# Kernel optimization log

Measured on AMD Instinct MI355X. Metric: run time of the kernel, lower is better.

## Reference

```python
import jax, jax.numpy as jnp
import numpy as np

N = 100000
E = 1600000
G = 256
D_IN = 128
NEURON = 64
ATT_F = 8
K = 3
ALPHA = 0.1


def setup_inputs() -> dict:
    key = jax.random.key(0)
    ks = jax.random.split(key, 12)
    x = jax.random.normal(ks[0], (N, D_IN), dtype=jnp.float32)
    closeness_feature = jax.random.normal(ks[1], (N, ATT_F), dtype=jnp.float32)
    edge_index = jax.random.randint(ks[2], (2, E), 0, N, dtype=jnp.int32)
    batch = jnp.sort(jax.random.randint(ks[3], (N,), 0, G, dtype=jnp.int32))
    s = 0.05
    return {
        "x": x,
        "closeness_feature": closeness_feature,
        "edge_index": edge_index,
        "batch": batch,
        "num_graphs": G,
        "nn1_w": jax.random.normal(ks[4], (D_IN, NEURON), dtype=jnp.float32) * s,
        "nn1_b": jnp.zeros((NEURON,), dtype=jnp.float32),
        "close_w": jax.random.normal(ks[5], (ATT_F, 1), dtype=jnp.float32) * s,
        "close_b": jnp.zeros((1,), dtype=jnp.float32),
        "att1_w": jax.random.normal(ks[6], (NEURON, 16), dtype=jnp.float32) * s,
        "att1_b": jnp.zeros((16,), dtype=jnp.float32),
        "att2_w": jax.random.normal(ks[7], (16, 1), dtype=jnp.float32) * s,
        "att2_b": jnp.zeros((1,), dtype=jnp.float32),
    }


def _appnp(x, edge_index, n):
    # gcn_norm with self-loops: A_hat = D^{-1/2}(A+I)D^{-1/2}
    loop = jnp.arange(n, dtype=edge_index.dtype)
    src = jnp.concatenate([edge_index[0], loop])
    dst = jnp.concatenate([edge_index[1], loop])
    deg = jax.ops.segment_sum(jnp.ones_like(dst, dtype=x.dtype), dst, num_segments=n)
    dinv = jax.lax.rsqrt(deg)  # deg >= 1 due to self loops
    norm = (dinv[src] * dinv[dst])[:, None]  # [E+N, 1]
    h = x
    for _ in range(K):
        agg = jax.ops.segment_sum(norm * h[src], dst, num_segments=n)
        h = (1.0 - ALPHA) * agg + ALPHA * x
    return h


def reference(x, closeness_feature, edge_index, batch, num_graphs,
              nn1_w, nn1_b, close_w, close_b, att1_w, att1_b, att2_w, att2_b):
    n = x.shape[0]
    h = _appnp(x, edge_index, n)                      # [N, D_IN]
    h = jax.nn.relu(h @ nn1_w + nn1_b)                # [N, 64]

    # per-graph softmax over closeness scores (segment softmax)
    logits = (closeness_feature @ close_w + close_b)[:, 0]          # [N]
    m = jax.ops.segment_max(logits, batch, num_segments=num_graphs)  # [G]
    w = jnp.exp(logits - m[batch])
    z = jax.ops.segment_sum(w, batch, num_segments=num_graphs)       # [G]
    p = w / z[batch]                                                 # softmax per graph

    cnt = jax.ops.segment_sum(jnp.ones((n,), dtype=h.dtype), batch,
                              num_segments=num_graphs)               # nodes per graph
    p = p * cnt[batch]                                               # scaled by curr_size

    # self_max: per-graph max over weighted node features
    pooled = jax.ops.segment_max(p[:, None] * h, batch, num_segments=num_graphs)  # [G, 64]

    a = jax.nn.relu(pooled @ att1_w + att1_b)         # [G, 16]
    return a @ att2_w + att2_b                        # [G, 1]
```

## Files before the change

kernel.cpp:

```cpp
#include <hip/hip_runtime.h>
#include <cstdint>
#include <cstddef>


#define DIN 128
#define NEU 64
#define BK2 512
#define BKSHIFT2 9
#define BKCAP 16384
#define ESCAP 12288
#define MAXNB 256

typedef __attribute__((ext_vector_type(8))) short short8v;
typedef __attribute__((ext_vector_type(4))) float f32x4;

__device__ inline float bf2f(unsigned short h) {
    return __uint_as_float(((unsigned)h) << 16);
}
__device__ inline unsigned short f2bf(float f) {
    unsigned u = __float_as_uint(f);
    unsigned r = u + 0x7FFFu + ((u >> 16) & 1u);
    return (unsigned short)(r >> 16);
}


__global__ __launch_bounds__(256) void binA_kernel(
        const int* __restrict__ src, const int* __restrict__ dst,
        int* __restrict__ bcur, int* __restrict__ pk, int E, int NB) {
    __shared__ int hist[MAXNB];
    __shared__ int cur[MAXNB];
    int nchunk = gridDim.x;
    int chunk = (E + nchunk - 1) / nchunk;
    int lo = blockIdx.x * chunk;
    int hi = min(E, lo + chunk);
    int t = threadIdx.x;
    for (int b = t; b < NB; b += 256) hist[b] = 0;
    __syncthreads();
    for (int i = lo + t; i < hi; i += 256)
        atomicAdd(&hist[dst[i] >> BKSHIFT2], 1);
    __syncthreads();
    for (int b = t; b < NB; b += 256)
        cur[b] = atomicAdd(&bcur[b], hist[b]);
    __syncthreads();
    for (int i = lo + t; i < hi; i += 256) {
        int d = dst[i];
        int b = d >> BKSHIFT2;
        int pos = atomicAdd(&cur[b], 1);
        pk[(size_t)b * BKCAP + pos] = (src[i] << BKSHIFT2) | (d & (BK2 - 1));
    }
}


__global__ void bscan_kernel(const int* __restrict__ bcur, int* __restrict__ bbase, int NB) {
    __shared__ int sh[256];
    int t = threadIdx.x;
    sh[t] = (t < NB) ? bcur[t] : 0;
    __syncthreads();
    for (int d = 1; d < 256; d <<= 1) {
        int v = (t >= d) ? sh[t - d] : 0;
        __syncthreads();
        sh[t] += v;
        __syncthreads();
    }
    if (t < NB) bbase[t + 1] = sh[t];
    if (t == 0) bbase[0] = 0;
}


__global__ __launch_bounds__(256) void binB_kernel(
        const int* __restrict__ bcur, const int* __restrict__ bbase,
        const int* __restrict__ pk, int* __restrict__ es,
        int* __restrict__ rowptr, float* __restrict__ dinv, int N, int NB) {
    __shared__ int cur[BK2];
    __shared__ int sh[256];
    __shared__ int esl[ESCAP];
    int b = blockIdx.x;
    int t = threadIdx.x;
    int node0 = b << BKSHIFT2;
    int count = bcur[b];
    int base = bbase[b];
    const int* pb = pk + (size_t)b * BKCAP;

    for (int v = t; v < BK2; v += 256) cur[v] = 0;
    __syncthreads();
    for (int i = t; i < count; i += 256)
        atomicAdd(&cur[pb[i] & (BK2 - 1)], 1);
    __syncthreads();
    int c0 = cur[2 * t], c1 = cur[2 * t + 1];
    int s = c0 + c1;
    sh[t] = s;
    __syncthreads();
    for (int d = 1; d < 256; d <<= 1) {
        int v = (t >= d) ? sh[t - d] : 0;
        __syncthreads();
        sh[t] += v;
        __syncthreads();
    }
    int excl = sh[t] - s;
    int n0 = node0 + 2 * t;
    if (n0 < N) {
        rowptr[n0 + 1] = base + excl + c0;
        dinv[n0] = rsqrtf((float)c0 + 1.0f);
    }
    if (n0 + 1 < N) {
        rowptr[n0 + 2] = base + excl + c0 + c1;
        dinv[n0 + 1] = rsqrtf((float)c1 + 1.0f);
    }
    if (b == 0 && t == 0) rowptr[0] = 0;
    __syncthreads();
    cur[2 * t] = excl;
    cur[2 * t + 1] = excl + c0;
    __syncthreads();
    for (int i = t; i < count; i += 256) {
        int v = pb[i];
        int pos = atomicAdd(&cur[v & (BK2 - 1)], 1);
        if (pos < ESCAP) esl[pos] = v >> BKSHIFT2;
    }
    __syncthreads();
    for (int i = t; i < count; i += 256) es[base + i] = esl[i];
}


__global__ __launch_bounds__(256) void fc1_kernel(
        const float* __restrict__ x, const float* __restrict__ W,
        ushort* __restrict__ yb, int N) {
    __shared__ ushort sW[DIN * NEU];
    int tid = threadIdx.x;
    for (int k = tid; k < DIN * NEU / 2; k += 256) {
        float2 v = ((const float2*)W)[k];
        ushort2 o;
        o.x = f2bf(v.x);
        o.y = f2bf(v.y);
        ((ushort2*)sW)[k] = o;
    }
    __syncthreads();
    int lane = tid & 63;
    int wv = tid >> 6;
    int l15 = lane & 15;
    int lg = lane >> 4;
    short8v bfrag[4][4];
#pragma unroll
    for (int kt = 0; kt < 4; kt++)
#pragma unroll
        for (int ct = 0; ct < 4; ct++) {
            short8v f;
#pragma unroll
            for (int e = 0; e < 8; e++)
                f[e] = (short)sW[(kt * 32 + lg * 8 + e) * NEU + ct * 16 + l15];
            bfrag[kt][ct] = f;
        }
    long long row0 = (long long)blockIdx.x * 64 + wv * 16;
    if (row0 >= N) return;
    bool rowok = (row0 + l15) < N;
    const float* xr = x + (size_t)(row0 + l15) * DIN;
    f32x4 acc[4];
#pragma unroll
    for (int ct = 0; ct < 4; ct++) acc[ct] = (f32x4){0.f, 0.f, 0.f, 0.f};
#pragma unroll
    for (int kt = 0; kt < 4; kt++) {
        short8v af = (short8v){0, 0, 0, 0, 0, 0, 0, 0};
        if (rowok) {
            float4 v0 = *((const float4*)(xr + kt * 32 + lg * 8));
            float4 v1 = *((const float4*)(xr + kt * 32 + lg * 8 + 4));
            af[0] = (short)f2bf(v0.x); af[1] = (short)f2bf(v0.y);
            af[2] = (short)f2bf(v0.z); af[3] = (short)f2bf(v0.w);
            af[4] = (short)f2bf(v1.x); af[5] = (short)f2bf(v1.y);
            af[6] = (short)f2bf(v1.z); af[7] = (short)f2bf(v1.w);
        }
#pragma unroll
        for (int ct = 0; ct < 4; ct++)
            acc[ct] = __builtin_amdgcn_mfma_f32_16x16x32_bf16(af, bfrag[kt][ct], acc[ct], 0, 0, 0);
    }
#pragma unroll
    for (int ct = 0; ct < 4; ct++)
#pragma unroll
        for (int r = 0; r < 4; r++) {
            long long rr = row0 + lg * 4 + r;
            if (rr < N) yb[(size_t)rr * NEU + ct * 16 + l15] = f2bf(acc[ct][r]);
        }
}


template <bool FINAL>
__global__ __launch_bounds__(256) void pull_kernel(
        const int* __restrict__ rowptr, const int* __restrict__ es,
        const float* __restrict__ dinv, const ushort* __restrict__ hin,
        const ushort* __restrict__ yb, const float* __restrict__ b1,
        ushort* __restrict__ hout, float* __restrict__ h2out, int N) {
    int wid = threadIdx.x >> 6;
    int lane = threadIdx.x & 63;
    int quarter = lane >> 4;
    int l16 = lane & 15;
    int node = blockIdx.x * 4 + wid;
    if (node >= N) return;
    int beg = rowptr[node], end = rowptr[node + 1];
    float dd = dinv[node];
    float4 acc0 = make_float4(0.f, 0.f, 0.f, 0.f);
    float4 acc1 = make_float4(0.f, 0.f, 0.f, 0.f);
    int deg = end - beg;
    for (int base = 0; base < deg; base += 64) {
        int myi = base + lane;
        int msrc = (myi < deg) ? es[beg + myi] : 0;
        float mns = (myi < deg) ? dinv[msrc] * dd : 0.f;
        int cnt = min(64, deg - base);
        int quads = (cnt + 3) >> 2;
        int j = 0;
        for (; j + 1 < quads; j += 2) {
            int i0 = 4 * j + quarter;
            int i1 = 4 * j + 4 + quarter;
            int s0 = __shfl(msrc, i0);
            float n0 = __shfl(mns, i0);
            int s1 = __shfl(msrc, i1);
            float n1 = __shfl(mns, i1);
            ushort4 w0 = *((const ushort4*)(hin + (size_t)s0 * NEU) + l16);
            ushort4 w1 = *((const ushort4*)(hin + (size_t)s1 * NEU) + l16);
            acc0.x = fmaf(n0, bf2f(w0.x), acc0.x);
            acc0.y = fmaf(n0, bf2f(w0.y), acc0.y);
            acc0.z = fmaf(n0, bf2f(w0.z), acc0.z);
            acc0.w = fmaf(n0, bf2f(w0.w), acc0.w);
            acc1.x = fmaf(n1, bf2f(w1.x), acc1.x);
            acc1.y = fmaf(n1, bf2f(w1.y), acc1.y);
            acc1.z = fmaf(n1, bf2f(w1.z), acc1.z);
            acc1.w = fmaf(n1, bf2f(w1.w), acc1.w);
        }
        if (j < quads) {
            int i0 = 4 * j + quarter;
            int s0 = __shfl(msrc, i0);
            float n0 = __shfl(mns, i0);
            ushort4 w0 = *((const ushort4*)(hin + (size_t)s0 * NEU) + l16);
            acc0.x = fmaf(n0, bf2f(w0.x), acc0.x);
            acc0.y = fmaf(n0, bf2f(w0.y), acc0.y);
            acc0.z = fmaf(n0, bf2f(w0.z), acc0.z);
            acc0.w = fmaf(n0, bf2f(w0.w), acc0.w);
        }
    }
    float4 acc;
    acc.x = acc0.x + acc1.x;
    acc.y = acc0.y + acc1.y;
    acc.z = acc0.z + acc1.z;
    acc.w = acc0.w + acc1.w;
    acc.x += __shfl_xor(acc.x, 16);
    acc.y += __shfl_xor(acc.y, 16);
    acc.z += __shfl_xor(acc.z, 16);
    acc.w += __shfl_xor(acc.w, 16);
    acc.x += __shfl_xor(acc.x, 32);
    acc.y += __shfl_xor(acc.y, 32);
    acc.z += __shfl_xor(acc.z, 32);
    acc.w += __shfl_xor(acc.w, 32);
    if (quarter == 0) {
        ushort4 hv = *((const ushort4*)(hin + (size_t)node * NEU) + l16);
        ushort4 xv = *((const ushort4*)(yb + (size_t)node * NEU) + l16);
        float d2 = dd * dd;
        float vx = 0.9f * (acc.x + d2 * bf2f(hv.x)) + 0.1f * bf2f(xv.x);
        float vy = 0.9f * (acc.y + d2 * bf2f(hv.y)) + 0.1f * bf2f(xv.y);
        float vz = 0.9f * (acc.z + d2 * bf2f(hv.z)) + 0.1f * bf2f(xv.z);
        float vw = 0.9f * (acc.w + d2 * bf2f(hv.w)) + 0.1f * bf2f(xv.w);
        if (FINAL) {
            float4 bb = *((const float4*)b1 + l16);
            float4 o;
            o.x = fmaxf(vx + bb.x, 0.f);
            o.y = fmaxf(vy + bb.y, 0.f);
            o.z = fmaxf(vz + bb.z, 0.f);
            o.w = fmaxf(vw + bb.w, 0.f);
            *((float4*)(h2out + (size_t)node * NEU) + l16) = o;
        } else {
            ushort4 o;
            o.x = f2bf(vx); o.y = f2bf(vy); o.z = f2bf(vz); o.w = f2bf(vw);
            *((ushort4*)(hout + (size_t)node * NEU) + l16) = o;
        }
    }
}


__global__ void logits_kernel(const float* __restrict__ cf, const float* __restrict__ cw,
                              const float* __restrict__ cb, float* __restrict__ logits, int N) {
    int i = blockIdx.x * blockDim.x + threadIdx.x;
    if (i >= N) return;
    const float4* c = (const float4*)(cf + (size_t)i * 8);
    float4 a = c[0], b = c[1];
    float s = a.x * cw[0] + a.y * cw[1] + a.z * cw[2] + a.w * cw[3]
            + b.x * cw[4] + b.y * cw[5] + b.z * cw[6] + b.w * cw[7] + cb[0];
    logits[i] = s;
}


__global__ void boundary_kernel(const int* __restrict__ batch, int* __restrict__ offs,
                                int N, int G) {
    int g = blockIdx.x * blockDim.x + threadIdx.x;
    if (g > G) return;
    int lo = 0, hi = N;
    while (lo < hi) {
        int mid = (lo + hi) >> 1;
        if (batch[mid] < g) lo = mid + 1; else hi = mid;
    }
    offs[g] = lo;
}


__global__ __launch_bounds__(256) void softmax_kernel(
        const float* __restrict__ logits, const int* __restrict__ offs,
        float* __restrict__ p, int G) {
    int g = blockIdx.x;
    int s0 = offs[g], e0 = offs[g + 1];
    int tid = threadIdx.x;
    __shared__ float red[256];
    float m = -INFINITY;
    for (int i = s0 + tid; i < e0; i += 256) m = fmaxf(m, logits[i]);
    red[tid] = m; __syncthreads();
    for (int w = 128; w > 0; w >>= 1) {
        if (tid < w) red[tid] = fmaxf(red[tid], red[tid + w]);
        __syncthreads();
    }
    m = red[0]; __syncthreads();
    float z = 0.f;
    for (int i = s0 + tid; i < e0; i += 256) z += expf(logits[i] - m);
    red[tid] = z; __syncthreads();
    for (int w = 128; w > 0; w >>= 1) {
        if (tid < w) red[tid] += red[tid + w];
        __syncthreads();
    }
    z = red[0];
    float scale = (float)(e0 - s0) / z;
    for (int i = s0 + tid; i < e0; i += 256) p[i] = expf(logits[i] - m) * scale;
}


__global__ __launch_bounds__(256) void pool_kernel(
        const float* __restrict__ h2, const float* __restrict__ p,
        const int* __restrict__ offs, float* __restrict__ pooled, int G) {
    int g = blockIdx.x;
    int s0 = offs[g], e0 = offs[g + 1];
    int tid = threadIdx.x;
    int j = tid & 63, r = tid >> 6;
    float mx = -INFINITY;
    for (int i = s0 + r; i < e0; i += 4)
        mx = fmaxf(mx, p[i] * h2[(size_t)i * NEU + j]);
    __shared__ float red[256];
    red[tid] = mx;
    __syncthreads();
    if (r == 0) {
        float m0 = fmaxf(fmaxf(red[j], red[64 + j]), fmaxf(red[128 + j], red[192 + j]));
        pooled[(size_t)g * NEU + j] = m0;
    }
}


__global__ void final_kernel(const float* __restrict__ pooled, const float* __restrict__ w1,
                             const float* __restrict__ b1, const float* __restrict__ w2,
                             const float* __restrict__ b2, float* __restrict__ out, int G) {
    int g = blockIdx.x;
    int tid = threadIdx.x;
    __shared__ float sp[64];
    __shared__ float sa[16];
    sp[tid] = pooled[(size_t)g * 64 + tid];
    __syncthreads();
    if (tid < 16) {
        float acc = b1[tid];
#pragma unroll
        for (int k = 0; k < 64; k++) acc = fmaf(sp[k], w1[k * 16 + tid], acc);
        sa[tid] = fmaxf(acc, 0.f);
    }
    __syncthreads();
    if (tid == 0) {
        float o = b2[0];
#pragma unroll
        for (int k = 0; k < 16; k++) o = fmaf(sa[k], w2[k], o);
        out[g] = o;
    }
}


extern "C" void kernel_launch(void* const* d_in, const int* in_sizes, int n_in,
                              void* d_out, int out_size, void* d_ws, size_t ws_size,
                              hipStream_t stream) {
    const float* x       = (const float*)d_in[0];
    const float* cf      = (const float*)d_in[1];
    const int*   ei      = (const int*)d_in[2];
    const int*   batch   = (const int*)d_in[3];
    const float* nn1_w   = (const float*)d_in[5];
    const float* nn1_b   = (const float*)d_in[6];
    const float* close_w = (const float*)d_in[7];
    const float* close_b = (const float*)d_in[8];
    const float* att1_w  = (const float*)d_in[9];
    const float* att1_b  = (const float*)d_in[10];
    const float* att2_w  = (const float*)d_in[11];
    const float* att2_b  = (const float*)d_in[12];
    float* out = (float*)d_out;

    int N = in_sizes[0] / DIN;
    int E = in_sizes[2] / 2;
    int G = out_size;

    const int* src = ei;
    const int* dst = ei + E;

    char* w = (char*)d_ws;
    size_t off = 0;
    auto alloc = [&](size_t bytes) -> void* {
        void* ptr = w + off;
        off += (bytes + 511) & ~(size_t)511;
        return ptr;
    };
    int NB = (N + BK2 - 1) >> BKSHIFT2;

    ushort* yb     = (ushort*)alloc((size_t)N * NEU * 2);
    ushort* hb0    = (ushort*)alloc((size_t)N * NEU * 2);
    ushort* hb1    = (ushort*)alloc((size_t)N * NEU * 2);
    float* h2      = (float*)alloc((size_t)N * NEU * 4);
    float* dinv    = (float*)alloc((size_t)N * 4);
    int*   rowptr  = (int*)alloc(((size_t)N + 1) * 4);
    int*   es      = (int*)alloc((size_t)E * 4);
    int*   bcur    = (int*)alloc((size_t)NB * 4);
    int*   bbase   = (int*)alloc(((size_t)NB + 1) * 4);
    int*   pk      = (int*)alloc((size_t)NB * BKCAP * 4);
    float* logits  = (float*)alloc((size_t)N * 4);
    float* p       = (float*)alloc((size_t)N * 4);
    int*   offs    = (int*)alloc(((size_t)G + 1) * 4);
    float* pooled  = (float*)alloc((size_t)G * NEU * 4);
    (void)ws_size; (void)n_in;

    hipMemsetAsync(bcur, 0, (size_t)NB * 4, stream);

    fc1_kernel<<<(N + 63) / 64, 256, 0, stream>>>(x, nn1_w, yb, N);

    binA_kernel<<<256, 256, 0, stream>>>(src, dst, bcur, pk, E, NB);
    bscan_kernel<<<1, 256, 0, stream>>>(bcur, bbase, NB);
    binB_kernel<<<NB, 256, 0, stream>>>(bcur, bbase, pk, es, rowptr, dinv, N, NB);

    pull_kernel<false><<<(N + 3) / 4, 256, 0, stream>>>(rowptr, es, dinv, yb,  yb, nn1_b, hb0, nullptr, N);
    pull_kernel<false><<<(N + 3) / 4, 256, 0, stream>>>(rowptr, es, dinv, hb0, yb, nn1_b, hb1, nullptr, N);
    pull_kernel<true ><<<(N + 3) / 4, 256, 0, stream>>>(rowptr, es, dinv, hb1, yb, nn1_b, nullptr, h2, N);

    logits_kernel<<<(N + 255) / 256, 256, 0, stream>>>(cf, close_w, close_b, logits, N);
    boundary_kernel<<<2, 256, 0, stream>>>(batch, offs, N, G);
    softmax_kernel<<<G, 256, 0, stream>>>(logits, offs, p, G);
    pool_kernel<<<G, 256, 0, stream>>>(h2, p, offs, pooled, G);
    final_kernel<<<G, 64, 0, stream>>>(pooled, att1_w, att1_b, att2_w, att2_b, out, G);
}
```

Baseline: 251.2 us.

## Prescale features by dinv so pull kernels skip per-edge norm gathers

Stores g = dinv*h instead of h, so each edge contribution becomes a plain sum of gathered rows, with dinv applied once per destination node. This removes the per-edge dinv[src] gather and the multiply. Padding with a zero sentinel row lets each wave unroll to four independent gathers per step without a tail branch. It adds a scale kernel and an extra buffer, and bf16 rounding now applies to the scaled values.

```diff
diff --git a/kernel.cpp b/kernel.cpp
--- a/kernel.cpp
+++ b/kernel.cpp
@@ -181,12 +181,37 @@
 }
 
 
-template <bool FINAL>
+__global__ void scale_kernel(const ushort* __restrict__ yb, const float* __restrict__ dinv,
+                             ushort* __restrict__ g0, ushort* __restrict__ g1,
+                             ushort* __restrict__ g2, int N) {
+    int i = blockIdx.x * blockDim.x + threadIdx.x;
+    int stride = gridDim.x * blockDim.x;
+    int total = N * 16;
+    for (; i < total; i += stride) {
+        int node = i >> 4;
+        float dd = dinv[node];
+        ushort4 v = ((const ushort4*)yb)[i];
+        ushort4 o;
+        o.x = f2bf(dd * bf2f(v.x));
+        o.y = f2bf(dd * bf2f(v.y));
+        o.z = f2bf(dd * bf2f(v.z));
+        o.w = f2bf(dd * bf2f(v.w));
+        ((ushort4*)g0)[i] = o;
+    }
+    if (blockIdx.x == 0 && threadIdx.x < 48) {
+        int buf = threadIdx.x >> 4, e = threadIdx.x & 15;
+        ushort* gp = (buf == 0) ? g0 : (buf == 1) ? g1 : g2;
+        ((ushort4*)(gp + (size_t)N * NEU))[e] = make_ushort4(0, 0, 0, 0);
+    }
+}
+
+
+template <int MODE>
 __global__ __launch_bounds__(256) void pull_kernel(
         const int* __restrict__ rowptr, const int* __restrict__ es,
-        const float* __restrict__ dinv, const ushort* __restrict__ hin,
+        const float* __restrict__ dinv, const ushort* __restrict__ gin,
         const ushort* __restrict__ yb, const float* __restrict__ b1,
-        ushort* __restrict__ hout, float* __restrict__ h2out, int N) {
+        ushort* __restrict__ gout, float* __restrict__ h2out, int N) {
     int wid = threadIdx.x >> 6;
     int lane = threadIdx.x & 63;
     int quarter = lane >> 4;
@@ -195,50 +220,37 @@
     if (node >= N) return;
     int beg = rowptr[node], end = rowptr[node + 1];
     float dd = dinv[node];
-    float4 acc0 = make_float4(0.f, 0.f, 0.f, 0.f);
-    float4 acc1 = make_float4(0.f, 0.f, 0.f, 0.f);
+    float4 a0 = make_float4(0.f, 0.f, 0.f, 0.f);
+    float4 a1 = make_float4(0.f, 0.f, 0.f, 0.f);
+    float4 a2 = make_float4(0.f, 0.f, 0.f, 0.f);
+    float4 a3 = make_float4(0.f, 0.f, 0.f, 0.f);
     int deg = end - beg;
     for (int base = 0; base < deg; base += 64) {
         int myi = base + lane;
-        int msrc = (myi < deg) ? es[beg + myi] : 0;
-        float mns = (myi < deg) ? dinv[msrc] * dd : 0.f;
+        int msrc = (myi < deg) ? es[beg + myi] : N;
         int cnt = min(64, deg - base);
-        int quads = (cnt + 3) >> 2;
-        int j = 0;
-        for (; j + 1 < quads; j += 2) {
-            int i0 = 4 * j + quarter;
-            int i1 = 4 * j + 4 + quarter;
+        int quads4 = (cnt + 15) >> 4;
+        for (int j = 0; j < quads4; j++) {
+            int i0 = 16 * j + quarter;
             int s0 = __shfl(msrc, i0);
-            float n0 = __shfl(mns, i0);
-            int s1 = __shfl(msrc, i1);
-            float n1 = __shfl(mns, i1);
-            ushort4 w0 = *((const ushort4*)(hin + (size_t)s0 * NEU) + l16);
-            ushort4 w1 = *((const ushort4*)(hin + (size_t)s1 * NEU) + l16);
-            acc0.x = fmaf(n0, bf2f(w0.x), acc0.x);
-            acc0.y = fmaf(n0, bf2f(w0.y), acc0.y);
-            acc0.z = fmaf(n0, bf2f(w0.z), acc0.z);
-            acc0.w = fmaf(n0, bf2f(w0.w), acc0.w);
-            acc1.x = fmaf(n1, bf2f(w1.x), acc1.x);
-            acc1.y = fmaf(n1, bf2f(w1.y), acc1.y);
-            acc1.z = fmaf(n1, bf2f(w1.z), acc1.z);
-            acc1.w = fmaf(n1, bf2f(w1.w), acc1.w);
+            int s1 = __shfl(msrc, i0 + 4);
+            int s2 = __shfl(msrc, i0 + 8);
+            int s3 = __shfl(msrc, i0 + 12);
+            ushort4 w0 = *((const ushort4*)(gin + (size_t)s0 * NEU) + l16);
+            ushort4 w1 = *((const ushort4*)(gin + (size_t)s1 * NEU) + l16);
+            ushort4 w2 = *((const ushort4*)(gin + (size_t)s2 * NEU) + l16);
+            ushort4 w3 = *((const ushort4*)(gin + (size_t)s3 * NEU) + l16);
+            a0.x += bf2f(w0.x); a0.y += bf2f(w0.y); a0.z += bf2f(w0.z); a0.w += bf2f(w0.w);
+            a1.x += bf2f(w1.x); a1.y += bf2f(w1.y); a1.z += bf2f(w1.z); a1.w += bf2f(w1.w);
+            a2.x += bf2f(w2.x); a2.y += bf2f(w2.y); a2.z += bf2f(w2.z); a2.w += bf2f(w2.w);
+            a3.x += bf2f(w3.x); a3.y += bf2f(w3.y); a3.z += bf2f(w3.z); a3.w += bf2f(w3.w);
         }
-        if (j < quads) {
-            int i0 = 4 * j + quarter;
-            int s0 = __shfl(msrc, i0);
-            float n0 = __shfl(mns, i0);
-            ushort4 w0 = *((const ushort4*)(hin + (size_t)s0 * NEU) + l16);
-            acc0.x = fmaf(n0, bf2f(w0.x), acc0.x);
-            acc0.y = fmaf(n0, bf2f(w0.y), acc0.y);
-            acc0.z = fmaf(n0, bf2f(w0.z), acc0.z);
-            acc0.w = fmaf(n0, bf2f(w0.w), acc0.w);
-        }
     }
     float4 acc;
-    acc.x = acc0.x + acc1.x;
-    acc.y = acc0.y + acc1.y;
-    acc.z = acc0.z + acc1.z;
-    acc.w = acc0.w + acc1.w;
+    acc.x = (a0.x + a1.x) + (a2.x + a3.x);
+    acc.y = (a0.y + a1.y) + (a2.y + a3.y);
+    acc.z = (a0.z + a1.z) + (a2.z + a3.z);
+    acc.w = (a0.w + a1.w) + (a2.w + a3.w);
     acc.x += __shfl_xor(acc.x, 16);
     acc.y += __shfl_xor(acc.y, 16);
     acc.z += __shfl_xor(acc.z, 16);
@@ -248,25 +260,26 @@
     acc.z += __shfl_xor(acc.z, 32);
     acc.w += __shfl_xor(acc.w, 32);
     if (quarter == 0) {
-        ushort4 hv = *((const ushort4*)(hin + (size_t)node * NEU) + l16);
-        ushort4 xv = *((const ushort4*)(yb + (size_t)node * NEU) + l16);
-        float d2 = dd * dd;
-        float vx = 0.9f * (acc.x + d2 * bf2f(hv.x)) + 0.1f * bf2f(xv.x);
-        float vy = 0.9f * (acc.y + d2 * bf2f(hv.y)) + 0.1f * bf2f(xv.y);
-        float vz = 0.9f * (acc.z + d2 * bf2f(hv.z)) + 0.1f * bf2f(xv.z);
-        float vw = 0.9f * (acc.w + d2 * bf2f(hv.w)) + 0.1f * bf2f(xv.w);
-        if (FINAL) {
+        ushort4 gv = *((const ushort4*)(gin + (size_t)node * NEU) + l16);
+        ushort4 yv = *((const ushort4*)(yb + (size_t)node * NEU) + l16);
+        float c9 = 0.9f * dd;
+        float hx = c9 * (acc.x + bf2f(gv.x)) + 0.1f * bf2f(yv.x);
+        float hy = c9 * (acc.y + bf2f(gv.y)) + 0.1f * bf2f(yv.y);
+        float hz = c9 * (acc.z + bf2f(gv.z)) + 0.1f * bf2f(yv.z);
+        float hw = c9 * (acc.w + bf2f(gv.w)) + 0.1f * bf2f(yv.w);
+        if (MODE == 1) {
             float4 bb = *((const float4*)b1 + l16);
             float4 o;
-            o.x = fmaxf(vx + bb.x, 0.f);
-            o.y = fmaxf(vy + bb.y, 0.f);
-            o.z = fmaxf(vz + bb.z, 0.f);
-            o.w = fmaxf(vw + bb.w, 0.f);
+            o.x = fmaxf(hx + bb.x, 0.f);
+            o.y = fmaxf(hy + bb.y, 0.f);
+            o.z = fmaxf(hz + bb.z, 0.f);
+            o.w = fmaxf(hw + bb.w, 0.f);
             *((float4*)(h2out + (size_t)node * NEU) + l16) = o;
         } else {
             ushort4 o;
-            o.x = f2bf(vx); o.y = f2bf(vy); o.z = f2bf(vz); o.w = f2bf(vw);
-            *((ushort4*)(hout + (size_t)node * NEU) + l16) = o;
+            o.x = f2bf(dd * hx); o.y = f2bf(dd * hy);
+            o.z = f2bf(dd * hz); o.w = f2bf(dd * hw);
+            *((ushort4*)(gout + (size_t)node * NEU) + l16) = o;
         }
     }
 }
@@ -404,8 +417,9 @@
     int NB = (N + BK2 - 1) >> BKSHIFT2;
 
     ushort* yb     = (ushort*)alloc((size_t)N * NEU * 2);
-    ushort* hb0    = (ushort*)alloc((size_t)N * NEU * 2);
-    ushort* hb1    = (ushort*)alloc((size_t)N * NEU * 2);
+    ushort* g0     = (ushort*)alloc(((size_t)N + 1) * NEU * 2);
+    ushort* g1     = (ushort*)alloc(((size_t)N + 1) * NEU * 2);
+    ushort* g2     = (ushort*)alloc(((size_t)N + 1) * NEU * 2);
     float* h2      = (float*)alloc((size_t)N * NEU * 4);
     float* dinv    = (float*)alloc((size_t)N * 4);
     int*   rowptr  = (int*)alloc(((size_t)N + 1) * 4);
@@ -421,15 +435,16 @@
 
     hipMemsetAsync(bcur, 0, (size_t)NB * 4, stream);
 
-    fc1_kernel<<<(N + 63) / 64, 256, 0, stream>>>(x, nn1_w, yb, N);
-
     binA_kernel<<<256, 256, 0, stream>>>(src, dst, bcur, pk, E, NB);
     bscan_kernel<<<1, 256, 0, stream>>>(bcur, bbase, NB);
     binB_kernel<<<NB, 256, 0, stream>>>(bcur, bbase, pk, es, rowptr, dinv, N, NB);
 
-    pull_kernel<false><<<(N + 3) / 4, 256, 0, stream>>>(rowptr, es, dinv, yb,  yb, nn1_b, hb0, nullptr, N);
-    pull_kernel<false><<<(N + 3) / 4, 256, 0, stream>>>(rowptr, es, dinv, hb0, yb, nn1_b, hb1, nullptr, N);
-    pull_kernel<true ><<<(N + 3) / 4, 256, 0, stream>>>(rowptr, es, dinv, hb1, yb, nn1_b, nullptr, h2, N);
+    fc1_kernel<<<(N + 63) / 64, 256, 0, stream>>>(x, nn1_w, yb, N);
+    scale_kernel<<<2048, 256, 0, stream>>>(yb, dinv, g0, g1, g2, N);
+
+    pull_kernel<0><<<(N + 3) / 4, 256, 0, stream>>>(rowptr, es, dinv, g0, yb, nn1_b, g1, nullptr, N);
+    pull_kernel<0><<<(N + 3) / 4, 256, 0, stream>>>(rowptr, es, dinv, g1, yb, nn1_b, g2, nullptr, N);
+    pull_kernel<1><<<(N + 3) / 4, 256, 0, stream>>>(rowptr, es, dinv, g2, yb, nn1_b, nullptr, h2, N);
 
     logits_kernel<<<(N + 255) / 256, 256, 0, stream>>>(cf, close_w, close_b, logits, N);
     boundary_kernel<<<2, 256, 0, stream>>>(batch, offs, N, G);
```

Result: faster. 239.5 us (-4.7%).
